# Kernel optimization log

Hardware: AMD Instinct MI355X
Metric: run time of the kernel (lower is better)

Reference implementation:

```python
import jax, jax.numpy as jnp
import numpy as np

N_NODES = 100000
N_EDGES = 50000
NNZ = 800000
D_IN = 128
D_OUT = 128


def setup_inputs() -> dict:
    key = jax.random.key(0)
    k1, k2, k3, k4, k5 = jax.random.split(key, 5)
    x_0 = jax.random.normal(k1, (N_NODES, D_IN), dtype=jnp.float32)
    W = jax.random.normal(k2, (D_OUT, D_IN), dtype=jnp.float32) / np.sqrt(D_IN)
    b = jax.random.normal(k3, (D_OUT,), dtype=jnp.float32) * 0.01
    node_ids = jax.random.randint(k4, (NNZ,), 0, N_NODES, dtype=jnp.int32)
    edge_ids = jax.random.randint(k5, (NNZ,), 0, N_EDGES, dtype=jnp.int32)
    return {"x_0": x_0, "W": W, "b": b, "node_ids": node_ids, "edge_ids": edge_ids}


def reference(x_0, W, b, node_ids, edge_ids):
    # Linear transform (no batchnorm: use_bn=False)
    x = x_0 @ W.T + b  # [n_nodes, out_channels]

    # Step 1: hyperedge aggregation (e_aggr='sum'):  m_{0->1} = B_1^T x, reduce=sum
    m01 = jax.ops.segment_sum(x[node_ids], edge_ids, num_segments=N_EDGES)  # [n_edges, d]

    # Step 2: node aggregation (v_aggr='mean'):  m_{1->0} = B_1 m_{0->1}, reduce=mean
    s = jax.ops.segment_sum(m01[edge_ids], node_ids, num_segments=N_NODES)  # [n_nodes, d]
    cnt = jax.ops.segment_sum(jnp.ones((NNZ,), dtype=x.dtype), node_ids, num_segments=N_NODES)
    m10 = s / jnp.maximum(cnt, 1.0)[:, None]

    # Step 3: SAGE update (residual add)
    return x + m10
```

## Files before the change

kernel.cpp:

```cpp
#include <hip/hip_runtime.h>
#include <hip/hip_bf16.h>

#define NN 100000
#define NE 50000
#define NZ 800000
#define D  128
#define NSEG (NE + NN)
#define FILL_P 4
#define FILL_B 782
#define G_GEMM 782
#define G_HIST 391

typedef __bf16 bf16x8 __attribute__((ext_vector_type(8)));
typedef float f32x4 __attribute__((ext_vector_type(4)));

static __device__ __forceinline__ unsigned short f2bf(float f) {
  union { float f; unsigned u; } v; v.f = f;
  unsigned r = (v.u + 0x7FFFu + ((v.u >> 16) & 1u)) >> 16;
  return (unsigned short)r;
}
static __device__ __forceinline__ float bf2f(unsigned short h) {
  union { unsigned u; float f; } v; v.u = ((unsigned)h) << 16;
  return v.f;
}

__global__ __launch_bounds__(256) void unisage_gemm_hist(const float* __restrict__ x0,
                                                         const float* __restrict__ W,
                                                         const float* __restrict__ bias,
                                                         unsigned short* __restrict__ xb,
                                                         const int* __restrict__ nid,
                                                         const int* __restrict__ eid,
                                                         int* __restrict__ cnt,
                                                         unsigned int* __restrict__ rank) {
  __shared__ __bf16 Wl[128][136];
  if (blockIdx.x < G_GEMM) {
    const int t = threadIdx.x;
#pragma unroll
    for (int i = 0; i < 16; ++i) {
      int idx = i * 1024 + t * 4;
      int dout = idx >> 7;
      int k = idx & 127;
      float4 wv = *(const float4*)(W + idx);
      Wl[dout][k + 0] = (__bf16)wv.x;
      Wl[dout][k + 1] = (__bf16)wv.y;
      Wl[dout][k + 2] = (__bf16)wv.z;
      Wl[dout][k + 3] = (__bf16)wv.w;
    }
    __syncthreads();

    const int wave = t >> 6;
    const int lane = t & 63;
    const int lr = lane & 15;
    const int lg = lane >> 4;
    const int rowbase = blockIdx.x * 128 + wave * 32;

    f32x4 acc[2][8] = {};

#pragma unroll
    for (int ks = 0; ks < 4; ++ks) {
      const int k0 = ks * 32 + lg * 8;
      bf16x8 b[8];
#pragma unroll
      for (int cf = 0; cf < 8; ++cf)
        b[cf] = *(const bf16x8*)&Wl[cf * 16 + lr][k0];
#pragma unroll
      for (int rf = 0; rf < 2; ++rf) {
        int row = rowbase + rf * 16 + lr;
        row = row < NN ? row : NN - 1;
        const float* src = x0 + (size_t)row * D + k0;
        float4 f0 = *(const float4*)(src);
        float4 f1 = *(const float4*)(src + 4);
        bf16x8 a;
        a[0] = (__bf16)f0.x; a[1] = (__bf16)f0.y;
        a[2] = (__bf16)f0.z; a[3] = (__bf16)f0.w;
        a[4] = (__bf16)f1.x; a[5] = (__bf16)f1.y;
        a[6] = (__bf16)f1.z; a[7] = (__bf16)f1.w;
#pragma unroll
        for (int cf = 0; cf < 8; ++cf)
          acc[rf][cf] = __builtin_amdgcn_mfma_f32_16x16x32_bf16(a, b[cf], acc[rf][cf], 0, 0, 0);
      }
    }

#pragma unroll
    for (int cf = 0; cf < 8; ++cf) {
      float bv = bias[cf * 16 + lr];
#pragma unroll
      for (int rf = 0; rf < 2; ++rf) {
#pragma unroll
        for (int r = 0; r < 4; ++r) {
          int row = rowbase + rf * 16 + lg * 4 + r;
          if (row < NN)
            xb[(size_t)row * D + cf * 16 + lr] = f2bf(acc[rf][cf][r] + bv);
        }
      }
    }
  } else {
    int base = ((blockIdx.x - G_GEMM) * 256 + threadIdx.x) * 8;
    if (base >= NZ) return;
    int4 ea = *(const int4*)(eid + base);
    int4 eb = *(const int4*)(eid + base + 4);
    int4 na = *(const int4*)(nid + base);
    int4 nb = *(const int4*)(nid + base + 4);
    int e[8] = {ea.x, ea.y, ea.z, ea.w, eb.x, eb.y, eb.z, eb.w};
    int v[8] = {na.x, na.y, na.z, na.w, nb.x, nb.y, nb.z, nb.w};
    unsigned re[8], rn[8];
#pragma unroll
    for (int j = 0; j < 8; ++j) re[j] = (unsigned)atomicAdd(&cnt[e[j]], 1);
#pragma unroll
    for (int j = 0; j < 8; ++j) rn[j] = (unsigned)atomicAdd(&cnt[NE + v[j]], 1);
    uint4 r0, r1;
    r0.x = (re[0] & 0xffffu) | (rn[0] << 16);
    r0.y = (re[1] & 0xffffu) | (rn[1] << 16);
    r0.z = (re[2] & 0xffffu) | (rn[2] << 16);
    r0.w = (re[3] & 0xffffu) | (rn[3] << 16);
    r1.x = (re[4] & 0xffffu) | (rn[4] << 16);
    r1.y = (re[5] & 0xffffu) | (rn[5] << 16);
    r1.z = (re[6] & 0xffffu) | (rn[6] << 16);
    r1.w = (re[7] & 0xffffu) | (rn[7] << 16);
    *(uint4*)(rank + base) = r0;
    *(uint4*)(rank + base + 4) = r1;
  }
}

__global__ void unisage_scan_k1(const int* __restrict__ in, int* __restrict__ bsum, int n) {
  __shared__ int sh[256];
  int t = threadIdx.x;
  int base = blockIdx.x * 1024 + t * 4;
  int s = 0;
#pragma unroll
  for (int j = 0; j < 4; ++j)
    if (base + j < n) s += in[base + j];
  sh[t] = s;
  __syncthreads();
  for (int o = 128; o > 0; o >>= 1) {
    if (t < o) sh[t] += sh[t + o];
    __syncthreads();
  }
  if (t == 0) bsum[blockIdx.x] = sh[0];
}

__global__ void unisage_scan_k3(const int* __restrict__ in, const int* __restrict__ bsum,
                                int* __restrict__ out, int n, int nb) {
  __shared__ int sh[256];
  int t = threadIdx.x;
  int bv = (t < nb) ? bsum[t] : 0;
  sh[t] = bv;
  __syncthreads();
  for (int o = 1; o < 256; o <<= 1) {
    int add = (t >= o) ? sh[t - o] : 0;
    __syncthreads();
    sh[t] += add;
    __syncthreads();
  }
  int bbase = (blockIdx.x == 0) ? 0 : sh[blockIdx.x - 1];
  __syncthreads();

  int base = blockIdx.x * 1024 + t * 4;
  int v[4];
#pragma unroll
  for (int j = 0; j < 4; ++j) v[j] = (base + j < n) ? in[base + j] : 0;
  int tsum = v[0] + v[1] + v[2] + v[3];
  sh[t] = tsum;
  __syncthreads();
  for (int o = 1; o < 256; o <<= 1) {
    int add = (t >= o) ? sh[t - o] : 0;
    __syncthreads();
    sh[t] += add;
    __syncthreads();
  }
  int run = sh[t] - tsum + bbase;
#pragma unroll
  for (int j = 0; j < 4; ++j) {
    if (base + j < n) out[base + j] = run;
    run += v[j];
  }
}

__global__ void unisage_fill(const int* __restrict__ nid, const int* __restrict__ eid,
                             const unsigned int* __restrict__ rank,
                             const int* __restrict__ off,
                             int* __restrict__ csr_e, int* __restrict__ csr_n) {
  const int R = (NSEG + FILL_P - 1) / FILL_P;
  int pass = blockIdx.x / FILL_B;
  int base = ((blockIdx.x % FILL_B) * 256 + threadIdx.x) * 4;
  if (base >= NZ) return;
  int lo = pass * R, hi = lo + R;
  int4 e4 = *(const int4*)(eid + base);
  int4 n4 = *(const int4*)(nid + base);
  uint4 r4 = *(const uint4*)(rank + base);
  int e[4] = {e4.x, e4.y, e4.z, e4.w};
  int v[4] = {n4.x, n4.y, n4.z, n4.w};
  unsigned r[4] = {r4.x, r4.y, r4.z, r4.w};
#pragma unroll
  for (int j = 0; j < 4; ++j) {
    if (e[j] >= lo && e[j] < hi) csr_e[off[e[j]] + (int)(r[j] & 0xffffu)] = v[j];
    int s = NE + v[j];
    if (s >= lo && s < hi) csr_n[off[s] + (int)(r[j] >> 16) - NZ] = e[j];
  }
}

#define QRED(x) { x += __shfl_xor(x, 16, 64); x += __shfl_xor(x, 32, 64); }

__global__ void unisage_edge_agg(const unsigned short* __restrict__ xb,
                                 const int* __restrict__ csr_e,
                                 const int* __restrict__ off, const int* __restrict__ cnt,
                                 unsigned short* __restrict__ m01b) {
  int w = (blockIdx.x * 256 + threadIdx.x) >> 6;
  int lane = threadIdx.x & 63;
  if (w >= NE) return;
  int quad = lane >> 4;
  int sl = lane & 15;
  int beg = off[w];
  int deg = cnt[w];
  int end = beg + deg;
  float a0 = 0, a1 = 0, a2 = 0, a3 = 0, a4 = 0, a5 = 0, a6 = 0, a7 = 0;
  for (int base = beg; base < end; base += 64) {
    int m = min(64, end - base);
    int idx = (lane < m) ? csr_e[base + lane] : 0;
    int iters = (m + 3) >> 2;
    for (int jj = 0; jj < iters; ++jj) {
      int p = 4 * jj + quad;
      int r = __shfl(idx, p, 64);
      if (p < m) {
        uint4 vv = *(const uint4*)(xb + (size_t)r * D + sl * 8);
        a0 += bf2f((unsigned short)(vv.x & 0xffffu)); a1 += bf2f((unsigned short)(vv.x >> 16));
        a2 += bf2f((unsigned short)(vv.y & 0xffffu)); a3 += bf2f((unsigned short)(vv.y >> 16));
        a4 += bf2f((unsigned short)(vv.z & 0xffffu)); a5 += bf2f((unsigned short)(vv.z >> 16));
        a6 += bf2f((unsigned short)(vv.w & 0xffffu)); a7 += bf2f((unsigned short)(vv.w >> 16));
      }
    }
  }
  QRED(a0) QRED(a1) QRED(a2) QRED(a3) QRED(a4) QRED(a5) QRED(a6) QRED(a7)
  if (quad == 0) {
    uint4 o;
    o.x = (unsigned)f2bf(a0) | ((unsigned)f2bf(a1) << 16);
    o.y = (unsigned)f2bf(a2) | ((unsigned)f2bf(a3) << 16);
    o.z = (unsigned)f2bf(a4) | ((unsigned)f2bf(a5) << 16);
    o.w = (unsigned)f2bf(a6) | ((unsigned)f2bf(a7) << 16);
    *(uint4*)(m01b + (size_t)w * D + sl * 8) = o;
  }
}

__global__ void unisage_node_agg(const unsigned short* __restrict__ xb,
                                 const unsigned short* __restrict__ m01b,
                                 const int* __restrict__ csr_n,
                                 const int* __restrict__ off, const int* __restrict__ cnt,
                                 float* __restrict__ out) {
  int w = (blockIdx.x * 256 + threadIdx.x) >> 6;
  int lane = threadIdx.x & 63;
  if (w >= NN) return;
  int quad = lane >> 4;
  int sl = lane & 15;
  int deg = cnt[NE + w];
  int beg = off[NE + w] - NZ;
  int end = beg + deg;
  float a0 = 0, a1 = 0, a2 = 0, a3 = 0, a4 = 0, a5 = 0, a6 = 0, a7 = 0;
  for (int base = beg; base < end; base += 64) {
    int m = min(64, end - base);
    int idx = (lane < m) ? csr_n[base + lane] : 0;
    int iters = (m + 3) >> 2;
    for (int jj = 0; jj < iters; ++jj) {
      int p = 4 * jj + quad;
      int r = __shfl(idx, p, 64);
      if (p < m) {
        uint4 vv = *(const uint4*)(m01b + (size_t)r * D + sl * 8);
        a0 += bf2f((unsigned short)(vv.x & 0xffffu)); a1 += bf2f((unsigned short)(vv.x >> 16));
        a2 += bf2f((unsigned short)(vv.y & 0xffffu)); a3 += bf2f((unsigned short)(vv.y >> 16));
        a4 += bf2f((unsigned short)(vv.z & 0xffffu)); a5 += bf2f((unsigned short)(vv.z >> 16));
        a6 += bf2f((unsigned short)(vv.w & 0xffffu)); a7 += bf2f((unsigned short)(vv.w >> 16));
      }
    }
  }
  QRED(a0) QRED(a1) QRED(a2) QRED(a3) QRED(a4) QRED(a5) QRED(a6) QRED(a7)
  if (quad == 0) {
    float inv = 1.0f / fmaxf((float)deg, 1.0f);
    uint4 xr = *(const uint4*)(xb + (size_t)w * D + sl * 8);
    float4 o0, o1;
    o0.x = bf2f((unsigned short)(xr.x & 0xffffu)) + a0 * inv;
    o0.y = bf2f((unsigned short)(xr.x >> 16))     + a1 * inv;
    o0.z = bf2f((unsigned short)(xr.y & 0xffffu)) + a2 * inv;
    o0.w = bf2f((unsigned short)(xr.y >> 16))     + a3 * inv;
    o1.x = bf2f((unsigned short)(xr.z & 0xffffu)) + a4 * inv;
    o1.y = bf2f((unsigned short)(xr.z >> 16))     + a5 * inv;
    o1.z = bf2f((unsigned short)(xr.w & 0xffffu)) + a6 * inv;
    o1.w = bf2f((unsigned short)(xr.w >> 16))     + a7 * inv;
    *(float4*)(out + (size_t)w * D + sl * 8) = o0;
    *(float4*)(out + (size_t)w * D + sl * 8 + 4) = o1;
  }
}

extern "C" void kernel_launch(void* const* d_in, const int* in_sizes, int n_in,
                              void* d_out, int out_size, void* d_ws, size_t ws_size,
                              hipStream_t stream) {
  const float* x0   = (const float*)d_in[0];
  const float* W    = (const float*)d_in[1];
  const float* bias = (const float*)d_in[2];
  const int* nid    = (const int*)d_in[3];
  const int* eid    = (const int*)d_in[4];
  float* out = (float*)d_out;

  unsigned short* xb   = (unsigned short*)d_ws;
  unsigned short* m01b = xb + (size_t)NN * D;
  int* cnt   = (int*)(m01b + (size_t)NE * D);
  int* off   = cnt + 150016;
  unsigned int* rank = (unsigned int*)(off + 150016);
  int* csr_e = (int*)(rank + NZ);
  int* csr_n = csr_e + NZ;
  int* bsum  = csr_n + NZ;

  hipMemsetAsync(cnt, 0, NSEG * sizeof(int), stream);

  unisage_gemm_hist<<<G_GEMM + G_HIST, 256, 0, stream>>>(x0, W, bias, xb, nid, eid, cnt, rank);

  const int nb = (NSEG + 1023) / 1024;
  unisage_scan_k1<<<nb, 256, 0, stream>>>(cnt, bsum, NSEG);
  unisage_scan_k3<<<nb, 256, 0, stream>>>(cnt, bsum, off, NSEG, nb);

  unisage_fill<<<FILL_P * FILL_B, 256, 0, stream>>>(nid, eid, rank, off, csr_e, csr_n);

  unisage_edge_agg<<<(NE * 64) / 256, 256, 0, stream>>>(xb, csr_e, off, cnt, m01b);
  unisage_node_agg<<<(NN * 64) / 256, 256, 0, stream>>>(xb, m01b, csr_n, off, cnt, out);
}
```

Baseline: 211.1 us.

## Split GEMM from histogram and partition atomic ranking into range passes

```diff
diff --git a/kernel.cpp b/kernel.cpp
--- a/kernel.cpp
+++ b/kernel.cpp
@@ -8,8 +8,10 @@
 #define NSEG (NE + NN)
 #define FILL_P 4
 #define FILL_B 782
-#define G_GEMM 782
-#define G_HIST 391
+#define HP 4
+#define HP_B 391
+#define RE_SZ 12500
+#define RN_SZ 25000
 
 typedef __bf16 bf16x8 __attribute__((ext_vector_type(8)));
 typedef float f32x4 __attribute__((ext_vector_type(4)));
@@ -24,102 +26,96 @@
   return v.f;
 }
 
-__global__ __launch_bounds__(256) void unisage_gemm_hist(const float* __restrict__ x0,
+__global__ __launch_bounds__(256) void unisage_gemm_mfma(const float* __restrict__ x0,
                                                          const float* __restrict__ W,
                                                          const float* __restrict__ bias,
-                                                         unsigned short* __restrict__ xb,
-                                                         const int* __restrict__ nid,
-                                                         const int* __restrict__ eid,
-                                                         int* __restrict__ cnt,
-                                                         unsigned int* __restrict__ rank) {
+                                                         unsigned short* __restrict__ xb) {
   __shared__ __bf16 Wl[128][136];
-  if (blockIdx.x < G_GEMM) {
-    const int t = threadIdx.x;
-#pragma unroll
-    for (int i = 0; i < 16; ++i) {
-      int idx = i * 1024 + t * 4;
-      int dout = idx >> 7;
-      int k = idx & 127;
-      float4 wv = *(const float4*)(W + idx);
-      Wl[dout][k + 0] = (__bf16)wv.x;
-      Wl[dout][k + 1] = (__bf16)wv.y;
-      Wl[dout][k + 2] = (__bf16)wv.z;
-      Wl[dout][k + 3] = (__bf16)wv.w;
+  const int t = threadIdx.x;
+#pragma unroll
+  for (int i = 0; i < 16; ++i) {
+    int idx = i * 1024 + t * 4;
+    int dout = idx >> 7;
+    int k = idx & 127;
+    float4 wv = *(const float4*)(W + idx);
+    Wl[dout][k + 0] = (__bf16)wv.x;
+    Wl[dout][k + 1] = (__bf16)wv.y;
+    Wl[dout][k + 2] = (__bf16)wv.z;
+    Wl[dout][k + 3] = (__bf16)wv.w;
+  }
+  __syncthreads();
+
+  const int wave = t >> 6;
+  const int lane = t & 63;
+  const int lr = lane & 15;
+  const int lg = lane >> 4;
+  const int rowbase = blockIdx.x * 128 + wave * 32;
+
+  f32x4 acc[2][8] = {};
+
+#pragma unroll
+  for (int ks = 0; ks < 4; ++ks) {
+    const int k0 = ks * 32 + lg * 8;
+    bf16x8 b[8];
+#pragma unroll
+    for (int cf = 0; cf < 8; ++cf)
+      b[cf] = *(const bf16x8*)&Wl[cf * 16 + lr][k0];
+#pragma unroll
+    for (int rf = 0; rf < 2; ++rf) {
+      int row = rowbase + rf * 16 + lr;
+      row = row < NN ? row : NN - 1;
+      const float* src = x0 + (size_t)row * D + k0;
+      float4 f0 = *(const float4*)(src);
+      float4 f1 = *(const float4*)(src + 4);
+      bf16x8 a;
+      a[0] = (__bf16)f0.x; a[1] = (__bf16)f0.y;
+      a[2] = (__bf16)f0.z; a[3] = (__bf16)f0.w;
+      a[4] = (__bf16)f1.x; a[5] = (__bf16)f1.y;
+      a[6] = (__bf16)f1.z; a[7] = (__bf16)f1.w;
+#pragma unroll
+      for (int cf = 0; cf < 8; ++cf)
+        acc[rf][cf] = __builtin_amdgcn_mfma_f32_16x16x32_bf16(a, b[cf], acc[rf][cf], 0, 0, 0);
     }
-    __syncthreads();
-
-    const int wave = t >> 6;
-    const int lane = t & 63;
-    const int lr = lane & 15;
-    const int lg = lane >> 4;
-    const int rowbase = blockIdx.x * 128 + wave * 32;
-
-    f32x4 acc[2][8] = {};
-
-#pragma unroll
-    for (int ks = 0; ks < 4; ++ks) {
-      const int k0 = ks * 32 + lg * 8;
-      bf16x8 b[8];
-#pragma unroll
-      for (int cf = 0; cf < 8; ++cf)
-        b[cf] = *(const bf16x8*)&Wl[cf * 16 + lr][k0];
-#pragma unroll
-      for (int rf = 0; rf < 2; ++rf) {
-        int row = rowbase + rf * 16 + lr;
-        row = row < NN ? row : NN - 1;
-        const float* src = x0 + (size_t)row * D + k0;
-        float4 f0 = *(const float4*)(src);
-        float4 f1 = *(const float4*)(src + 4);
-        bf16x8 a;
-        a[0] = (__bf16)f0.x; a[1] = (__bf16)f0.y;
-        a[2] = (__bf16)f0.z; a[3] = (__bf16)f0.w;
-        a[4] = (__bf16)f1.x; a[5] = (__bf16)f1.y;
-        a[6] = (__bf16)f1.z; a[7] = (__bf16)f1.w;
-#pragma unroll
-        for (int cf = 0; cf < 8; ++cf)
-          acc[rf][cf] = __builtin_amdgcn_mfma_f32_16x16x32_bf16(a, b[cf], acc[rf][cf], 0, 0, 0);
+  }
+
+#pragma unroll
+  for (int cf = 0; cf < 8; ++cf) {
+    float bv = bias[cf * 16 + lr];
+#pragma unroll
+    for (int rf = 0; rf < 2; ++rf) {
+#pragma unroll
+      for (int r = 0; r < 4; ++r) {
+        int row = rowbase + rf * 16 + lg * 4 + r;
+        if (row < NN)
+          xb[(size_t)row * D + cf * 16 + lr] = f2bf(acc[rf][cf][r] + bv);
       }
     }
-
-#pragma unroll
-    for (int cf = 0; cf < 8; ++cf) {
-      float bv = bias[cf * 16 + lr];
-#pragma unroll
-      for (int rf = 0; rf < 2; ++rf) {
-#pragma unroll
-        for (int r = 0; r < 4; ++r) {
-          int row = rowbase + rf * 16 + lg * 4 + r;
-          if (row < NN)
-            xb[(size_t)row * D + cf * 16 + lr] = f2bf(acc[rf][cf][r] + bv);
-        }
-      }
-    }
-  } else {
-    int base = ((blockIdx.x - G_GEMM) * 256 + threadIdx.x) * 8;
-    if (base >= NZ) return;
-    int4 ea = *(const int4*)(eid + base);
-    int4 eb = *(const int4*)(eid + base + 4);
-    int4 na = *(const int4*)(nid + base);
-    int4 nb = *(const int4*)(nid + base + 4);
-    int e[8] = {ea.x, ea.y, ea.z, ea.w, eb.x, eb.y, eb.z, eb.w};
-    int v[8] = {na.x, na.y, na.z, na.w, nb.x, nb.y, nb.z, nb.w};
-    unsigned re[8], rn[8];
-#pragma unroll
-    for (int j = 0; j < 8; ++j) re[j] = (unsigned)atomicAdd(&cnt[e[j]], 1);
-#pragma unroll
-    for (int j = 0; j < 8; ++j) rn[j] = (unsigned)atomicAdd(&cnt[NE + v[j]], 1);
-    uint4 r0, r1;
-    r0.x = (re[0] & 0xffffu) | (rn[0] << 16);
-    r0.y = (re[1] & 0xffffu) | (rn[1] << 16);
-    r0.z = (re[2] & 0xffffu) | (rn[2] << 16);
-    r0.w = (re[3] & 0xffffu) | (rn[3] << 16);
-    r1.x = (re[4] & 0xffffu) | (rn[4] << 16);
-    r1.y = (re[5] & 0xffffu) | (rn[5] << 16);
-    r1.z = (re[6] & 0xffffu) | (rn[6] << 16);
-    r1.w = (re[7] & 0xffffu) | (rn[7] << 16);
-    *(uint4*)(rank + base) = r0;
-    *(uint4*)(rank + base + 4) = r1;
-  }
+  }
+}
+
+__global__ void unisage_hist_rank(const int* __restrict__ nid, const int* __restrict__ eid,
+                                  int* __restrict__ cnt,
+                                  unsigned short* __restrict__ rank_e,
+                                  unsigned short* __restrict__ rank_n) {
+  int pass = blockIdx.x / HP_B;
+  int base = ((blockIdx.x % HP_B) * 256 + threadIdx.x) * 8;
+  if (base >= NZ) return;
+  int elo = pass * RE_SZ, ehi = elo + RE_SZ;
+  int vlo = pass * RN_SZ, vhi = vlo + RN_SZ;
+  int4 ea = *(const int4*)(eid + base);
+  int4 eb = *(const int4*)(eid + base + 4);
+  int4 na = *(const int4*)(nid + base);
+  int4 nb = *(const int4*)(nid + base + 4);
+  int e[8] = {ea.x, ea.y, ea.z, ea.w, eb.x, eb.y, eb.z, eb.w};
+  int v[8] = {na.x, na.y, na.z, na.w, nb.x, nb.y, nb.z, nb.w};
+#pragma unroll
+  for (int j = 0; j < 8; ++j)
+    if (e[j] >= elo && e[j] < ehi)
+      rank_e[base + j] = (unsigned short)atomicAdd(&cnt[e[j]], 1);
+#pragma unroll
+  for (int j = 0; j < 8; ++j)
+    if (v[j] >= vlo && v[j] < vhi)
+      rank_n[base + j] = (unsigned short)atomicAdd(&cnt[NE + v[j]], 1);
 }
 
 __global__ void unisage_scan_k1(const int* __restrict__ in, int* __restrict__ bsum, int n) {
@@ -177,7 +173,8 @@
 }
 
 __global__ void unisage_fill(const int* __restrict__ nid, const int* __restrict__ eid,
-                             const unsigned int* __restrict__ rank,
+                             const unsigned short* __restrict__ rank_e,
+                             const unsigned short* __restrict__ rank_n,
                              const int* __restrict__ off,
                              int* __restrict__ csr_e, int* __restrict__ csr_n) {
   const int R = (NSEG + FILL_P - 1) / FILL_P;
@@ -187,15 +184,17 @@
   int lo = pass * R, hi = lo + R;
   int4 e4 = *(const int4*)(eid + base);
   int4 n4 = *(const int4*)(nid + base);
-  uint4 r4 = *(const uint4*)(rank + base);
+  ushort4 re4 = *(const ushort4*)(rank_e + base);
+  ushort4 rn4 = *(const ushort4*)(rank_n + base);
   int e[4] = {e4.x, e4.y, e4.z, e4.w};
   int v[4] = {n4.x, n4.y, n4.z, n4.w};
-  unsigned r[4] = {r4.x, r4.y, r4.z, r4.w};
+  unsigned short re[4] = {re4.x, re4.y, re4.z, re4.w};
+  unsigned short rn[4] = {rn4.x, rn4.y, rn4.z, rn4.w};
 #pragma unroll
   for (int j = 0; j < 4; ++j) {
-    if (e[j] >= lo && e[j] < hi) csr_e[off[e[j]] + (int)(r[j] & 0xffffu)] = v[j];
+    if (e[j] >= lo && e[j] < hi) csr_e[off[e[j]] + (int)re[j]] = v[j];
     int s = NE + v[j];
-    if (s >= lo && s < hi) csr_n[off[s] + (int)(r[j] >> 16) - NZ] = e[j];
+    if (s >= lo && s < hi) csr_n[off[s] + (int)rn[j] - NZ] = e[j];
   }
 }
 
@@ -303,20 +302,23 @@
   unsigned short* m01b = xb + (size_t)NN * D;
   int* cnt   = (int*)(m01b + (size_t)NE * D);
   int* off   = cnt + 150016;
-  unsigned int* rank = (unsigned int*)(off + 150016);
-  int* csr_e = (int*)(rank + NZ);
+  unsigned short* rank_e = (unsigned short*)(off + 150016);
+  unsigned short* rank_n = rank_e + NZ;
+  int* csr_e = (int*)(rank_n + NZ);
   int* csr_n = csr_e + NZ;
   int* bsum  = csr_n + NZ;
 
   hipMemsetAsync(cnt, 0, NSEG * sizeof(int), stream);
 
-  unisage_gemm_hist<<<G_GEMM + G_HIST, 256, 0, stream>>>(x0, W, bias, xb, nid, eid, cnt, rank);
+  unisage_hist_rank<<<HP * HP_B, 256, 0, stream>>>(nid, eid, cnt, rank_e, rank_n);
+
+  unisage_gemm_mfma<<<(NN + 127) / 128, 256, 0, stream>>>(x0, W, bias, xb);
 
   const int nb = (NSEG + 1023) / 1024;
   unisage_scan_k1<<<nb, 256, 0, stream>>>(cnt, bsum, NSEG);
   unisage_scan_k3<<<nb, 256, 0, stream>>>(cnt, bsum, off, NSEG, nb);
 
-  unisage_fill<<<FILL_P * FILL_B, 256, 0, stream>>>(nid, eid, rank, off, csr_e, csr_n);
+  unisage_fill<<<FILL_P * FILL_B, 256, 0, stream>>>(nid, eid, rank_e, rank_n, off, csr_e, csr_n);
 
   unisage_edge_agg<<<(NE * 64) / 256, 256, 0, stream>>>(xb, csr_e, off, cnt, m01b);
   unisage_node_agg<<<(NN * 64) / 256, 256, 0, stream>>>(xb, m01b, csr_n, off, cnt, out);
```

Measured after the change: 237.7 us. 1.13x slower.
